# Kernel optimization log

Measured on AMD Instinct MI355X. Metric: run time of the kernel, lower is better.

Reference implementation:

```python
import jax, jax.numpy as jnp
import numpy as np

B, N_HEADS, F_TOK = 8, 12, 768
GRID_H, GRID_W = 32, 32
N_TOK = 1 + GRID_H * GRID_W  # 1025 (readout token + patches)
F_HEAD = F_TOK // N_HEADS    # 64
NUM_DIST = (2 * GRID_H - 1) * (2 * GRID_W - 1) + 3  # 3972


def _build_relpos_index(gh, gw):
    # BEiT-style relative position index with 3 extra slots for the readout token
    coords = np.stack(np.meshgrid(np.arange(gh), np.arange(gw), indexing='ij'))  # (2, gh, gw)
    flat = coords.reshape(2, -1)                                                 # (2, gh*gw)
    rel = flat[:, :, None] - flat[:, None, :]                                    # (2, P, P)
    rel = rel.transpose(1, 2, 0).astype(np.int64)                                # (P, P, 2)
    rel[:, :, 0] += gh - 1
    rel[:, :, 1] += gw - 1
    rel[:, :, 0] *= 2 * gw - 1
    rpi = rel.sum(-1)                                                            # (P, P)
    n = 1 + gh * gw
    nd = (2 * gh - 1) * (2 * gw - 1) + 3
    idx = np.zeros((n, n), dtype=np.int32)
    idx[1:, 1:] = rpi
    idx[0, :] = nd - 3  # readout -> all
    idx[:, 0] = nd - 2  # all -> readout
    idx[0, 0] = nd - 1  # readout -> readout
    return idx


def setup_inputs() -> dict:
    key = jax.random.key(0)
    ks = jax.random.split(key, 7)
    tokens = jax.random.normal(ks[0], (B, N_TOK, F_TOK), dtype=jnp.float32)
    qkv_w = jax.random.normal(ks[1], (3 * F_TOK, F_TOK), dtype=jnp.float32) * 0.02
    q_bias = jax.random.normal(ks[2], (1, N_HEADS, 1, F_HEAD), dtype=jnp.float32) * 0.02
    v_bias = jax.random.normal(ks[3], (1, N_HEADS, 1, F_HEAD), dtype=jnp.float32) * 0.02
    relpos_table = jax.random.normal(ks[4], (NUM_DIST, N_HEADS), dtype=jnp.float32) * 0.02
    proj_w = jax.random.normal(ks[5], (F_TOK, F_TOK), dtype=jnp.float32) * 0.02
    proj_b = jax.random.normal(ks[6], (F_TOK,), dtype=jnp.float32) * 0.02
    relpos_index = jnp.asarray(_build_relpos_index(GRID_H, GRID_W))  # (N, N) int32
    return {
        'tokens': tokens, 'qkv_w': qkv_w, 'q_bias': q_bias, 'v_bias': v_bias,
        'relpos_table': relpos_table, 'proj_w': proj_w, 'proj_b': proj_b,
        'relpos_index': relpos_index, 'patch_h': GRID_H, 'patch_w': GRID_W,
    }


def reference(tokens, qkv_w, q_bias, v_bias, relpos_table, proj_w, proj_b,
              relpos_index, patch_h, patch_w):
    b, n, f_tok = tokens.shape
    # qkv projection (no bias): (B, N, 3F) -> (3, B, H, N, f)
    qkv = tokens @ qkv_w.T
    qkv = qkv.reshape(b, n, 3, N_HEADS, F_HEAD).transpose(2, 0, 3, 1, 4)
    q, k, v = qkv[0], qkv[1], qkv[2]
    q = (q + q_bias) * (F_HEAD ** -0.5)
    v = v + v_bias
    # attention scores: (B, H, N, N)
    attn = jnp.einsum('bhnf,bhmf->bhnm', q, k)
    # relative position bias gather: (N, N, H) -> (H, N, N)
    bias = relpos_table[relpos_index].transpose(2, 0, 1)
    attn = attn + bias[None]
    w = jax.nn.softmax(attn, axis=-1)
    out = jnp.einsum('bhnm,bhmf->bhnf', w, v)
    out = out.transpose(0, 2, 1, 3).reshape(b, n, N_HEADS * F_HEAD)
    return out @ proj_w.T + proj_b
```

## Files before the change

kernel.cpp:

```cpp
#include <hip/hip_runtime.h>

#define B_ 8
#define NH 12
#define NTOK 1025
#define FT 768
#define MROWS (B_*NTOK)
#define NPAD2 1088
#define CH 17
#define NQT 36
#define NTT 34
#define NRT9 9

typedef __bf16 bf16x8 __attribute__((ext_vector_type(8)));
typedef __bf16 bf16x2 __attribute__((ext_vector_type(2)));
typedef float floatx4 __attribute__((ext_vector_type(4)));
typedef float floatx16 __attribute__((ext_vector_type(16)));
typedef int intx4 __attribute__((ext_vector_type(4)));

__device__ __forceinline__ void async_ld16(const void* gp, void* lp) {
  __builtin_amdgcn_global_load_lds(
      (const __attribute__((address_space(1))) void*)gp,
      (__attribute__((address_space(3))) void*)lp, 16, 0, 0);
}

__global__ void zero_ws(uint4* __restrict__ p, size_t n) {
  size_t i = (size_t)blockIdx.x * blockDim.x + threadIdx.x;
  size_t stride = (size_t)gridDim.x * blockDim.x;
  for (; i < n; i += stride) p[i] = make_uint4(0u, 0u, 0u, 0u);
}

__global__ __launch_bounds__(256) void cvt_bf16(const float* __restrict__ src,
                                                __bf16* __restrict__ dst, int n4) {
  int i = blockIdx.x * 256 + threadIdx.x;
  if (i >= n4) return;
  float4 v = ((const float4*)src)[i];
  __bf16 o[4] = {(__bf16)v.x, (__bf16)v.y, (__bf16)v.z, (__bf16)v.w};
  *(uint2*)(dst + 4 * (size_t)i) = *(uint2*)o;
}

__global__ __launch_bounds__(256) void bias_gather_t(
    const int* __restrict__ idx, const float* __restrict__ table,
    __bf16* __restrict__ Bb) {
  const int qt = blockIdx.x, tt = blockIdx.y;
  const int t = threadIdx.x;
  const int lane = t & 63, w = t >> 6;
  const int l31 = lane & 31, hb = lane >> 5;
  int qrow = qt * 32 + l31; if (qrow > NTOK - 1) qrow = NTOK - 1;
  int ids[16]; bool ok[16];
#pragma unroll
  for (int j = 0; j < 16; ++j) {
    const int token = tt * 32 + (j & 3) + 8 * (j >> 2) + 4 * hb;
    ok[j] = token < NTOK;
    ids[j] = ok[j] ? idx[qrow * NTOK + token] : 0;
  }
#pragma unroll
  for (int g = 0; g < 3; ++g) {
    const int h = w + g * 4;
    __bf16 v[16];
#pragma unroll
    for (int j = 0; j < 16; ++j)
      v[j] = ok[j] ? (__bf16)table[ids[j] * NH + h] : (__bf16)(-1e30f);
    uint4* dst = (uint4*)(Bb + (((size_t)h * NQT + qt) * NTT + tt) * 1024 + lane * 16);
    dst[0] = ((uint4*)v)[0];
    dst[1] = ((uint4*)v)[1];
  }
}

__device__ __forceinline__ void gemm128_core(
    const __bf16* __restrict__ A, const __bf16* __restrict__ W,
    int m0, int n0, int M, __bf16* At, __bf16* Bt, floatx4 acc[4][4]) {
  const int tid = threadIdx.x, wave = tid >> 6, lane = tid & 63;
  const int l = lane & 15, qd = lane >> 4;
  const int wr = wave >> 1, wc = wave & 1;
  const int srow = lane >> 2, sg = lane & 3;
  const int r0 = wave * 32 + srow;
  const int r1 = r0 + 16;
  int gm0 = m0 + r0; if (gm0 >= M) gm0 = M - 1;
  int gm1 = m0 + r1; if (gm1 >= M) gm1 = M - 1;
  const int sw0 = (sg ^ (r0 & 3)) * 8;
  const __bf16* gA0 = A + (size_t)gm0 * FT + sw0;
  const __bf16* gA1 = A + (size_t)gm1 * FT + sw0;
  const __bf16* gB0 = W + (size_t)(n0 + r0) * FT + sw0;
  const __bf16* gB1 = W + (size_t)(n0 + r1) * FT + sw0;
  __bf16* lA0 = At + (wave * 32) * 32;
  __bf16* lA1 = At + (wave * 32 + 16) * 32;
  __bf16* lB0 = Bt + (wave * 32) * 32;
  __bf16* lB1 = Bt + (wave * 32 + 16) * 32;
  const int fsw = (qd ^ (l & 3)) * 8;
  for (int k0 = 0; k0 < FT; k0 += 32) {
    async_ld16(gA0 + k0, lA0);
    async_ld16(gA1 + k0, lA1);
    async_ld16(gB0 + k0, lB0);
    async_ld16(gB1 + k0, lB1);
    __syncthreads();
    bf16x8 aF[4], bF[4];
#pragma unroll
    for (int t = 0; t < 4; ++t)
      aF[t] = *(const bf16x8*)(At + (wr * 64 + t * 16 + l) * 32 + fsw);
#pragma unroll
    for (int u = 0; u < 4; ++u)
      bF[u] = *(const bf16x8*)(Bt + (wc * 64 + u * 16 + l) * 32 + fsw);
#pragma unroll
    for (int t = 0; t < 4; ++t)
#pragma unroll
      for (int u = 0; u < 4; ++u)
        acc[t][u] = __builtin_amdgcn_mfma_f32_16x16x32_bf16(aF[t], bF[u], acc[t][u], 0, 0, 0);
    __syncthreads();
  }
}

__global__ __launch_bounds__(256) void qkv_gemm128(
    const __bf16* __restrict__ tokens, const __bf16* __restrict__ qkvw,
    const float* __restrict__ qbias, const float* __restrict__ vbias,
    __bf16* __restrict__ Qb, __bf16* __restrict__ Kc, __bf16* __restrict__ Vc) {
  __shared__ __bf16 At[128 * 32], Bt[128 * 32];
  const int tid = threadIdx.x, wave = tid >> 6, lane = tid & 63;
  const int l = lane & 15, qd = lane >> 4;
  const int wr = wave >> 1, wc = wave & 1;
  const int m0 = blockIdx.x * 128, n0 = blockIdx.y * 128;
  floatx4 acc[4][4];
#pragma unroll
  for (int t = 0; t < 4; ++t)
#pragma unroll
    for (int u = 0; u < 4; ++u) acc[t][u] = (floatx4){0.f, 0.f, 0.f, 0.f};
  gemm128_core(tokens, qkvw, m0, n0, MROWS, At, Bt, acc);

  const int which = (n0 / FT);
  const int nrem0 = n0 - which * FT;
#pragma unroll
  for (int u = 0; u < 4; ++u) {
    const int rem = nrem0 + wc * 64 + u * 16 + l;
    const int h = rem >> 6, f = rem & 63;
    const float qb = (which == 0) ? qbias[h * 64 + f] : 0.f;
    const float vb = (which == 2) ? vbias[h * 64 + f] : 0.f;
#pragma unroll
    for (int t = 0; t < 4; ++t) {
#pragma unroll
      for (int r = 0; r < 4; ++r) {
        const int gm = m0 + wr * 64 + t * 16 + qd * 4 + r;
        if (gm >= MROWS) continue;
        const int b = gm / NTOK;
        const int tok = gm - b * NTOK;
        const size_t bh = (size_t)(b * NH + h);
        float v = acc[t][u][r];
        if (which == 0) {
          Qb[(bh * NPAD2 + tok) * 64 + f] = (__bf16)((v + qb) * 0.125f);
        } else if (which == 1) {
          const size_t e = ((size_t)(bh * CH + (tok >> 6))) * 4096 +
                           (((f >> 3) * 64 + (tok & 63)) << 3) + (f & 7);
          Kc[e] = (__bf16)v;
        } else {
          const size_t e = ((size_t)(bh * CH + (tok >> 6))) * 4096 +
                           (((((tok >> 3) & 7) * 64 + f)) << 3) + (tok & 7);
          Vc[e] = (__bf16)(v + vb);
        }
      }
    }
  }
}

__global__ __launch_bounds__(256) void proj_gemm128(
    const __bf16* __restrict__ Ao, const __bf16* __restrict__ projw,
    const float* __restrict__ projb, float* __restrict__ out) {
  __shared__ __bf16 At[128 * 32], Bt[128 * 32];
  const int tid = threadIdx.x, wave = tid >> 6, lane = tid & 63;
  const int l = lane & 15, qd = lane >> 4;
  const int wr = wave >> 1, wc = wave & 1;
  const int m0 = blockIdx.x * 128, n0 = blockIdx.y * 128;
  floatx4 acc[4][4];
#pragma unroll
  for (int t = 0; t < 4; ++t)
#pragma unroll
    for (int u = 0; u < 4; ++u) acc[t][u] = (floatx4){0.f, 0.f, 0.f, 0.f};
  gemm128_core(Ao, projw, m0, n0, MROWS, At, Bt, acc);
#pragma unroll
  for (int u = 0; u < 4; ++u) {
    const int gn = n0 + wc * 64 + u * 16 + l;
    const float pb = projb[gn];
#pragma unroll
    for (int t = 0; t < 4; ++t)
#pragma unroll
      for (int r = 0; r < 4; ++r) {
        const int gm = m0 + wr * 64 + t * 16 + qd * 4 + r;
        if (gm < MROWS) out[(size_t)gm * FT + gn] = acc[t][u][r] + pb;
      }
  }
}

__global__ __launch_bounds__(256, 3) void attn_flash(
    const __bf16* __restrict__ Qb, const __bf16* __restrict__ Kc,
    const __bf16* __restrict__ Vc, const __bf16* __restrict__ Bb,
    __bf16* __restrict__ Ao) {
  __shared__ __bf16 Kl[4096], Vl[4096];
  const int bid = blockIdx.x;
  const int rt = bid % NRT9;
  const int bh = bid / NRT9;
  const int h = bh % NH, b = bh / NH;
  const int wave = threadIdx.x >> 6, lane = threadIdx.x & 63;
  const int l31 = lane & 31, hb = lane >> 5;
  const int qt = rt * 4 + wave;
  int qrow = qt * 32 + l31; if (qrow > NTOK - 1) qrow = NTOK - 1;

  bf16x8 qf[4];
  {
    const __bf16* Qp = Qb + ((size_t)bh * NPAD2 + qrow) * 64 + hb * 8;
#pragma unroll
    for (int d = 0; d < 4; ++d) qf[d] = *(const bf16x8*)(Qp + d * 16);
  }

  floatx16 o0, o1;
#pragma unroll
  for (int j = 0; j < 16; ++j) { o0[j] = 0.f; o1[j] = 0.f; }
  float lsum = 0.f;

  const __bf16* Kg = Kc + (size_t)bh * CH * 4096;
  const __bf16* Vg = Vc + (size_t)bh * CH * 4096;
  const __bf16* Bg = Bb + ((size_t)h * NQT + qt) * NTT * 1024 + lane * 16;

  for (int c = 0; c < CH; ++c) {
    {
      const __bf16* gk = Kg + c * 4096;
      const __bf16* gv = Vg + c * 4096;
#pragma unroll
      for (int ii = 0; ii < 4; ++ii) {
        const int i = wave * 4 + ii;
        const __bf16* src = (i < 8) ? (gk + i * 512) : (gv + (i - 8) * 512);
        __bf16* dst = (i < 8) ? (Kl + i * 512) : (Vl + (i - 8) * 512);
        async_ld16(src + lane * 8, dst);
      }
    }
    __syncthreads();

    int pk[2][8];
#pragma unroll
    for (int tt = 0; tt < 2; ++tt) {
      floatx16 st;
#pragma unroll
      for (int j = 0; j < 16; ++j) st[j] = 0.f;
#pragma unroll
      for (int dk = 0; dk < 4; ++dk) {
        bf16x8 a = *(const bf16x8*)(Kl + (((dk * 2 + hb) * 64) + tt * 32 + l31) * 8);
        st = __builtin_amdgcn_mfma_f32_32x32x16_bf16(a, qf[dk], st, 0, 0, 0);
      }
      bf16x8 b0 = *(const bf16x8*)(Bg + (size_t)(c * 2 + tt) * 1024);
      bf16x8 b1 = *(const bf16x8*)(Bg + (size_t)(c * 2 + tt) * 1024 + 8);
      float e[16];
#pragma unroll
      for (int j = 0; j < 16; ++j) {
        const float bj = (float)(j < 8 ? b0[j] : b1[j - 8]);
        e[j] = __expf(st[j] + bj);
        lsum += e[j];
      }
#pragma unroll
      for (int j2 = 0; j2 < 8; ++j2) {
        bf16x2 pr = {(__bf16)e[2 * j2], (__bf16)e[2 * j2 + 1]};
        pk[tt][j2] = __builtin_bit_cast(int, pr);
      }
    }

#pragma unroll
    for (int ks = 0; ks < 4; ++ks) {
      const int s = ks & 1, tt = ks >> 1;
      const int r01a = pk[tt][4 * s + 0], r01b = pk[tt][4 * s + 1];
      const int r23a = pk[tt][4 * s + 2], r23b = pk[tt][4 * s + 3];
      const int t01a = __shfl_xor(r01a, 32), t01b = __shfl_xor(r01b, 32);
      const int t23a = __shfl_xor(r23a, 32), t23b = __shfl_xor(r23b, 32);
      intx4 fi;
      fi[0] = hb ? t23a : r01a;
      fi[1] = hb ? t23b : r01b;
      fi[2] = hb ? r23a : t01a;
      fi[3] = hb ? r23b : t01b;
      bf16x8 pb = __builtin_bit_cast(bf16x8, fi);
      bf16x8 va0 = *(const bf16x8*)(Vl + (((ks * 2 + hb) * 64) + l31) * 8);
      bf16x8 va1 = *(const bf16x8*)(Vl + (((ks * 2 + hb) * 64) + 32 + l31) * 8);
      o0 = __builtin_amdgcn_mfma_f32_32x32x16_bf16(va0, pb, o0, 0, 0, 0);
      o1 = __builtin_amdgcn_mfma_f32_32x32x16_bf16(va1, pb, o1, 0, 0, 0);
    }
    __syncthreads();
  }

  const float ltot = lsum + __shfl_xor(lsum, 32);
  const float rinv = 1.0f / ltot;
  const int tok = rt * 128 + wave * 32 + l31;
  if (tok < NTOK) {
    __bf16* op = Ao + ((size_t)b * NTOK + tok) * FT + h * 64;
#pragma unroll
    for (int ft = 0; ft < 2; ++ft) {
#pragma unroll
      for (int jg = 0; jg < 4; ++jg) {
        const int f = ft * 32 + jg * 8 + hb * 4;
        __bf16 v4[4];
#pragma unroll
        for (int q = 0; q < 4; ++q) {
          const float ov = ft ? o1[jg * 4 + q] : o0[jg * 4 + q];
          v4[q] = (__bf16)(ov * rinv);
        }
        *(uint2*)(op + f) = *(uint2*)v4;
      }
    }
  }
}

extern "C" void kernel_launch(void* const* d_in, const int* in_sizes, int n_in,
                              void* d_out, int out_size, void* d_ws, size_t ws_size,
                              hipStream_t stream) {
  (void)in_sizes; (void)n_in; (void)out_size; (void)ws_size;
  const float* tokens = (const float*)d_in[0];
  const float* qkvw   = (const float*)d_in[1];
  const float* qbias  = (const float*)d_in[2];
  const float* vbias  = (const float*)d_in[3];
  const float* table  = (const float*)d_in[4];
  const float* projw  = (const float*)d_in[5];
  const float* projb  = (const float*)d_in[6];
  const int*   rpidx  = (const int*)d_in[7];
  float* out = (float*)d_out;
  char* ws = (char*)d_ws;

  const size_t QB2 = (size_t)B_ * NH * NPAD2 * 64 * 2;
  const size_t BBT = (size_t)NH * NQT * NTT * 1024 * 2;
  const size_t AOB = (size_t)MROWS * FT * 2;
  const size_t WQB = (size_t)3 * FT * FT * 2;
  __bf16* Qb = (__bf16*)(ws);
  __bf16* Kc = (__bf16*)(ws + QB2);
  __bf16* Vc = (__bf16*)(ws + 2 * QB2);
  __bf16* Bb = (__bf16*)(ws + 3 * QB2);
  __bf16* Tb = (__bf16*)(ws + 3 * QB2 + BBT);
  __bf16* Ao = Tb;
  __bf16* Wq = (__bf16*)(ws + 3 * QB2 + BBT + AOB);
  __bf16* Wp = (__bf16*)(ws + 3 * QB2 + BBT + AOB + WQB);

  zero_ws<<<1024, 256, 0, stream>>>((uint4*)(ws + QB2), (2 * QB2) / 16);
  cvt_bf16<<<(MROWS * FT / 4 + 255) / 256, 256, 0, stream>>>(tokens, Tb, MROWS * FT / 4);
  cvt_bf16<<<(3 * FT * FT / 4 + 255) / 256, 256, 0, stream>>>(qkvw, Wq, 3 * FT * FT / 4);
  cvt_bf16<<<(FT * FT / 4 + 255) / 256, 256, 0, stream>>>(projw, Wp, FT * FT / 4);
  bias_gather_t<<<dim3(NQT, NTT), 256, 0, stream>>>(rpidx, table, Bb);
  qkv_gemm128<<<dim3(65, 18), 256, 0, stream>>>(Tb, Wq, qbias, vbias, Qb, Kc, Vc);
  attn_flash<<<B_ * NH * NRT9, 256, 0, stream>>>(Qb, Kc, Vc, Bb, Ao);
  proj_gemm128<<<dim3(65, 6), 256, 0, stream>>>(Ao, Wp, projb, out);
}
```

Measured before the change: 302.8 us.

## Triple-buffer GEMM LDS loads with async prefetch and drop workspace zeroing

Replaces the synchronous load-then-compute loop in the shared GEMM core with a 3-stage ring of LDS buffers. The next k-tile is prefetched via global_load_lds while the current one is computed, with only one barrier per step. The aim is to hide global load latency behind MFMA work in the QKV and projection GEMMs. It also removes the kernel that zeroed the K/V workspace, which relies on padded entries being harmless. The trade-off is more LDS per block and a possible occupancy drop.

```diff
diff --git a/kernel.cpp b/kernel.cpp
--- a/kernel.cpp
+++ b/kernel.cpp
@@ -23,12 +23,6 @@
       (__attribute__((address_space(3))) void*)lp, 16, 0, 0);
 }
 
-__global__ void zero_ws(uint4* __restrict__ p, size_t n) {
-  size_t i = (size_t)blockIdx.x * blockDim.x + threadIdx.x;
-  size_t stride = (size_t)gridDim.x * blockDim.x;
-  for (; i < n; i += stride) p[i] = make_uint4(0u, 0u, 0u, 0u);
-}
-
 __global__ __launch_bounds__(256) void cvt_bf16(const float* __restrict__ src,
                                                 __bf16* __restrict__ dst, int n4) {
   int i = blockIdx.x * 256 + threadIdx.x;
@@ -66,15 +60,14 @@
   }
 }
 
-__device__ __forceinline__ void gemm128_core(
+__device__ __forceinline__ void gemm128_pipe(
     const __bf16* __restrict__ A, const __bf16* __restrict__ W,
     int m0, int n0, int M, __bf16* At, __bf16* Bt, floatx4 acc[4][4]) {
   const int tid = threadIdx.x, wave = tid >> 6, lane = tid & 63;
   const int l = lane & 15, qd = lane >> 4;
   const int wr = wave >> 1, wc = wave & 1;
   const int srow = lane >> 2, sg = lane & 3;
-  const int r0 = wave * 32 + srow;
-  const int r1 = r0 + 16;
+  const int r0 = wave * 32 + srow, r1 = r0 + 16;
   int gm0 = m0 + r0; if (gm0 >= M) gm0 = M - 1;
   int gm1 = m0 + r1; if (gm1 >= M) gm1 = M - 1;
   const int sw0 = (sg ^ (r0 & 3)) * 8;
@@ -82,38 +75,53 @@
   const __bf16* gA1 = A + (size_t)gm1 * FT + sw0;
   const __bf16* gB0 = W + (size_t)(n0 + r0) * FT + sw0;
   const __bf16* gB1 = W + (size_t)(n0 + r1) * FT + sw0;
-  __bf16* lA0 = At + (wave * 32) * 32;
-  __bf16* lA1 = At + (wave * 32 + 16) * 32;
-  __bf16* lB0 = Bt + (wave * 32) * 32;
-  __bf16* lB1 = Bt + (wave * 32 + 16) * 32;
+  const int woff = wave * 32 * 32;
   const int fsw = (qd ^ (l & 3)) * 8;
-  for (int k0 = 0; k0 < FT; k0 += 32) {
-    async_ld16(gA0 + k0, lA0);
-    async_ld16(gA1 + k0, lA1);
-    async_ld16(gB0 + k0, lB0);
-    async_ld16(gB1 + k0, lB1);
-    __syncthreads();
+
+  auto issue = [&](int k, int buf) {
+    __bf16* a = At + buf * 4096 + woff;
+    __bf16* b = Bt + buf * 4096 + woff;
+    async_ld16(gA0 + k * 32, a);
+    async_ld16(gA1 + k * 32, a + 512);
+    async_ld16(gB0 + k * 32, b);
+    async_ld16(gB1 + k * 32, b + 512);
+  };
+  auto step = [&](int buf) {
+    __builtin_amdgcn_s_barrier();
+    const __bf16* ab = At + buf * 4096;
+    const __bf16* bb = Bt + buf * 4096;
     bf16x8 aF[4], bF[4];
 #pragma unroll
     for (int t = 0; t < 4; ++t)
-      aF[t] = *(const bf16x8*)(At + (wr * 64 + t * 16 + l) * 32 + fsw);
+      aF[t] = *(const bf16x8*)(ab + (wr * 64 + t * 16 + l) * 32 + fsw);
 #pragma unroll
     for (int u = 0; u < 4; ++u)
-      bF[u] = *(const bf16x8*)(Bt + (wc * 64 + u * 16 + l) * 32 + fsw);
+      bF[u] = *(const bf16x8*)(bb + (wc * 64 + u * 16 + l) * 32 + fsw);
 #pragma unroll
     for (int t = 0; t < 4; ++t)
 #pragma unroll
       for (int u = 0; u < 4; ++u)
         acc[t][u] = __builtin_amdgcn_mfma_f32_16x16x32_bf16(aF[t], bF[u], acc[t][u], 0, 0, 0);
-    __syncthreads();
-  }
+  };
+
+  issue(0, 0);
+  int bk = 0;
+  for (int k = 0; k < 23; ++k) {
+    int bn = bk + 1; if (bn == 3) bn = 0;
+    issue(k + 1, bn);
+    __builtin_amdgcn_s_waitcnt(0x0F74);
+    step(bk);
+    bk = bn;
+  }
+  __builtin_amdgcn_s_waitcnt(0x0F70);
+  step(bk);
 }
 
 __global__ __launch_bounds__(256) void qkv_gemm128(
     const __bf16* __restrict__ tokens, const __bf16* __restrict__ qkvw,
     const float* __restrict__ qbias, const float* __restrict__ vbias,
     __bf16* __restrict__ Qb, __bf16* __restrict__ Kc, __bf16* __restrict__ Vc) {
-  __shared__ __bf16 At[128 * 32], Bt[128 * 32];
+  __shared__ __bf16 At[3 * 4096], Bt[3 * 4096];
   const int tid = threadIdx.x, wave = tid >> 6, lane = tid & 63;
   const int l = lane & 15, qd = lane >> 4;
   const int wr = wave >> 1, wc = wave & 1;
@@ -123,7 +131,7 @@
   for (int t = 0; t < 4; ++t)
 #pragma unroll
     for (int u = 0; u < 4; ++u) acc[t][u] = (floatx4){0.f, 0.f, 0.f, 0.f};
-  gemm128_core(tokens, qkvw, m0, n0, MROWS, At, Bt, acc);
+  gemm128_pipe(tokens, qkvw, m0, n0, MROWS, At, Bt, acc);
 
   const int which = (n0 / FT);
   const int nrem0 = n0 - which * FT;
@@ -162,7 +170,7 @@
 __global__ __launch_bounds__(256) void proj_gemm128(
     const __bf16* __restrict__ Ao, const __bf16* __restrict__ projw,
     const float* __restrict__ projb, float* __restrict__ out) {
-  __shared__ __bf16 At[128 * 32], Bt[128 * 32];
+  __shared__ __bf16 At[3 * 4096], Bt[3 * 4096];
   const int tid = threadIdx.x, wave = tid >> 6, lane = tid & 63;
   const int l = lane & 15, qd = lane >> 4;
   const int wr = wave >> 1, wc = wave & 1;
@@ -172,7 +180,7 @@
   for (int t = 0; t < 4; ++t)
 #pragma unroll
     for (int u = 0; u < 4; ++u) acc[t][u] = (floatx4){0.f, 0.f, 0.f, 0.f};
-  gemm128_core(Ao, projw, m0, n0, MROWS, At, Bt, acc);
+  gemm128_pipe(Ao, projw, m0, n0, MROWS, At, Bt, acc);
 #pragma unroll
   for (int u = 0; u < 4; ++u) {
     const int gn = n0 + wc * 64 + u * 16 + l;
@@ -329,7 +337,6 @@
   __bf16* Wq = (__bf16*)(ws + 3 * QB2 + BBT + AOB);
   __bf16* Wp = (__bf16*)(ws + 3 * QB2 + BBT + AOB + WQB);
 
-  zero_ws<<<1024, 256, 0, stream>>>((uint4*)(ws + QB2), (2 * QB2) / 16);
   cvt_bf16<<<(MROWS * FT / 4 + 255) / 256, 256, 0, stream>>>(tokens, Tb, MROWS * FT / 4);
   cvt_bf16<<<(3 * FT * FT / 4 + 255) / 256, 256, 0, stream>>>(qkvw, Wq, 3 * FT * FT / 4);
   cvt_bf16<<<(FT * FT / 4 + 255) / 256, 256, 0, stream>>>(projw, Wp, FT * FT / 4);
```

New measurement: 298.8 us. Within noise of the previous version (-1.3%).
